# Performance work log

Hardware: AMD Instinct MI355X
Metric: run time of the kernel (lower is better)

## Reference

```python
import jax, jax.numpy as jnp
import numpy as np

RADIUS = 2                 # soft detection radius (init kwarg)
NMS_RADIUS = 2             # hardcoded in detect_keypoints: simple_nms(scores, 2)
TOP_K = 4096
TEMPERATURE = 0.1
KSIZE = 2 * RADIUS + 1     # 5
KK = KSIZE * KSIZE         # 25


def _hw_grid(dtype):
    # flatten order j = dy*KSIZE + dx ; entry = (x_off, y_off)  (torch's [:, [1,0]])
    lin = jnp.linspace(-RADIUS, RADIUS, KSIZE, dtype=dtype)
    gx, gy = jnp.meshgrid(lin, lin)  # 'xy': gx[dy,dx]=lin[dx], gy[dy,dx]=lin[dy]
    return jnp.stack([gx, gy], axis=-1).reshape(-1, 2)  # (KK, 2)


def _maxpool(x, r):
    k = 2 * r + 1
    return jax.lax.reduce_window(x, -jnp.inf, jax.lax.max,
                                 (1, 1, k, k), (1, 1, 1, 1),
                                 ((0, 0), (0, 0), (r, r), (r, r)))


def _simple_nms(scores, r):
    zeros = jnp.zeros_like(scores)
    max_mask = scores == _maxpool(scores, r)
    for _ in range(2):
        supp_mask = _maxpool(max_mask.astype(scores.dtype), r) > 0
        supp_scores = jnp.where(supp_mask, zeros, scores)
        new_max_mask = supp_scores == _maxpool(supp_scores, r)
        max_mask = max_mask | (new_max_mask & ~supp_mask)
    return jnp.where(max_mask, scores, zeros)


def _bilinear_zeros(img, xy):
    # img: (h, w); xy: (K, 2) normalized [-1,1]; align_corners=True, zero padding
    h, w = img.shape
    px = (xy[:, 0] + 1.0) * 0.5 * (w - 1)
    py = (xy[:, 1] + 1.0) * 0.5 * (h - 1)
    x0 = jnp.floor(px); y0 = jnp.floor(py)
    wx1 = px - x0; wx0 = 1.0 - wx1
    wy1 = py - y0; wy0 = 1.0 - wy1
    def tap(xi, yi, wgt):
        valid = (xi >= 0) & (xi < w) & (yi >= 0) & (yi < h)
        xc = jnp.clip(xi, 0, w - 1).astype(jnp.int32)
        yc = jnp.clip(yi, 0, h - 1).astype(jnp.int32)
        return jnp.where(valid, img[yc, xc], 0.0) * wgt
    return (tap(x0, y0, wx0 * wy0) + tap(x0 + 1, y0, wx1 * wy0)
            + tap(x0, y0 + 1, wx0 * wy1) + tap(x0 + 1, y0 + 1, wx1 * wy1))


def _dkd_forward(scores_map):
    b, c, h, w = scores_map.shape
    dtype = scores_map.dtype
    scores_nograd = jax.lax.stop_gradient(scores_map)

    nms_scores = _simple_nms(scores_nograd, NMS_RADIUS)
    # zero out border band of width RADIUS
    ybad = (jnp.arange(h) < RADIUS) | (jnp.arange(h) >= h - RADIUS)
    xbad = (jnp.arange(w) < RADIUS) | (jnp.arange(w) >= w - RADIUS)
    border = ybad[:, None] | xbad[None, :]
    nms_scores = jnp.where(border[None, None], 0.0, nms_scores)

    # top-k over flattened score map (per image)
    _, idx = jax.lax.top_k(nms_scores.reshape(b, -1), TOP_K)  # (b, K)
    ix = idx % w
    iy = idx // w

    # patch gather == unfold(scores_map) + gather, done sparsely with zero pad
    padded = jnp.pad(scores_map[:, 0], ((0, 0), (RADIUS, RADIUS), (RADIUS, RADIUS)))
    off = jnp.arange(KSIZE)
    ys = iy[:, :, None] + off[None, None, :]           # (b, K, KSIZE)
    xs = ix[:, :, None] + off[None, None, :]
    bidx = jnp.arange(b)[:, None, None, None]
    patch_scores = padded[bidx, ys[:, :, :, None], xs[:, :, None, :]]  # (b,K,KSIZE,KSIZE)
    patch_scores = patch_scores.reshape(b, TOP_K, KK)

    hw_grid = _hw_grid(dtype)                          # (KK, 2)
    max_v = jax.lax.stop_gradient(patch_scores.max(axis=-1, keepdims=True))
    x_exp = jnp.exp((patch_scores - max_v) / TEMPERATURE)   # (b,K,KK)
    x_exp_sum = x_exp.sum(axis=-1, keepdims=True)            # (b,K,1)
    xy_residual = jnp.einsum('bkp,pd->bkd', x_exp, hw_grid) / x_exp_sum  # (b,K,2)
    hw_dist2 = (((hw_grid[None, None] - xy_residual[:, :, None]) / RADIUS) ** 2).sum(-1)
    scoredispersity = (x_exp * hw_dist2).sum(-1) / x_exp_sum[..., 0]     # (b,K)

    keypoints_xy_nms = jnp.stack([ix, iy], axis=-1).astype(dtype)
    wh = jnp.array([w - 1, h - 1], dtype=dtype)
    keypoints_xy = (keypoints_xy_nms + xy_residual) / wh * 2.0 - 1.0     # (b,K,2)

    kptscore = jax.vmap(_bilinear_zeros)(scores_map[:, 0], keypoints_xy)  # (b,K)
    return keypoints_xy, kptscore, scoredispersity


def setup_inputs() -> dict:
    key = jax.random.key(0)
    scores_map = jax.random.uniform(key, (8, 1, 1024, 1024), dtype=jnp.float32)
    return {"scores_map": scores_map}


def reference(scores_map):
    # matches torch forward: (keypoints, kptscores, scoredispersitys)
    return _dkd_forward(scores_map)
```

## Files before the change

### kernel.cpp

```cpp
#include <hip/hip_runtime.h>
#include <stdint.h>

namespace {

constexpr int B = 8;
constexpr int H = 1024;
constexpr int W = 1024;
constexpr int TOPK = 4096;
constexpr int CAND_CAP = 131072;
constexpr int SEL_CAP = 16384;
constexpr int LIST_CAP = 320;
constexpr int HIST_N = 32768;
constexpr int NCHUNK = 32;
constexpr int NHB = 48;

constexpr int RROWS = 92;
constexpr int NG = 22;
constexpr int STR = 88;
constexpr int MW4 = 4;
constexpr int NSTRIP = 11;
constexpr int NUNIT = NG * NSTRIP;

constexpr int RK_ME = 256;
constexpr int RK_CH = 1024;

constexpr size_t OFF_CNT   = 0;
constexpr size_t OFF_GHIST = 4096;
constexpr size_t OFF_RANK  = OFF_GHIST + (size_t)B * HIST_N * 4;
constexpr size_t OFF_SEL   = OFF_RANK + (size_t)B * SEL_CAP * 4;
constexpr size_t OFF_TOPK  = OFF_SEL + (size_t)B * SEL_CAP * 8;
constexpr size_t OFF_CAND  = OFF_TOPK + (size_t)B * TOPK * 8;
constexpr size_t MEMSET_BYTES = OFF_RANK + (size_t)B * SEL_CAP * 4;

__device__ __forceinline__ float max5(float a, float b, float c, float d, float e) {
  return fmaxf(fmaxf(fmaxf(a, b), fmaxf(c, d)), e);
}
__device__ __forceinline__ float4 ld4(const float* p) {
  return *reinterpret_cast<const float4*>(p);
}

template <int PASS>
__device__ __forceinline__ void score_pass(
    int u, int x0, int y0, const float* __restrict__ S,
    const uint32_t* __restrict__ SUP, uint32_t* __restrict__ MA,
    uint64_t* list, uint32_t* cnt_loc, uint64_t* cand, uint32_t* cand_count, int b) {
  const int G = u % NG, s = u / NG;
  const int r0 = 2 + 8 * s;
  const int gx0 = x0 - 12 + 4 * G;
  uint32_t colm = 0;
#pragma unroll
  for (int j = 0; j < 4; ++j)
    if ((unsigned)(gx0 + j) < (unsigned)W) colm |= 1u << j;
  const int p = 4 * G - 4;
  const int pw = (p < 0) ? 0 : (p >> 5);
  const int psh = (p < 0) ? 0 : (p & 31);
  const int pls = (p < 0) ? -p : 0;

  float4 hw[5], cw[5];
  uint32_t sn[5];
#pragma unroll
  for (int k = 0; k < 12; ++k) {
    const int rr = r0 - 2 + k;
    const float* rowp = S + rr * STR + 4 * G;
    float4 d = ld4(rowp);
    float4 a = (G > 0) ? ld4(rowp - 4) : d;
    float4 e = (G < NG - 1) ? ld4(rowp + 4) : d;
    uint32_t supn = 0;
    if (PASS != 0) {
      const uint32_t* srow = SUP + rr * MW4;
      uint64_t X = (uint64_t)srow[pw] | ((uint64_t)srow[pw + 1] << 32);
      uint64_t win = pls ? (X << pls) : (X >> psh);
      if (win & 0x001u) a.x = 0.f;
      if (win & 0x002u) a.y = 0.f;
      if (win & 0x004u) a.z = 0.f;
      if (win & 0x008u) a.w = 0.f;
      if (win & 0x010u) d.x = 0.f;
      if (win & 0x020u) d.y = 0.f;
      if (win & 0x040u) d.z = 0.f;
      if (win & 0x080u) d.w = 0.f;
      if (win & 0x100u) e.x = 0.f;
      if (win & 0x200u) e.y = 0.f;
      if (win & 0x400u) e.z = 0.f;
      if (win & 0x800u) e.w = 0.f;
      supn = (uint32_t)(win >> 4) & 0xFu;
    }
    float4 hm;
    hm.x = max5(a.z, a.w, d.x, d.y, d.z);
    hm.y = max5(a.w, d.x, d.y, d.z, d.w);
    hm.z = max5(d.x, d.y, d.z, d.w, e.x);
    hm.w = max5(d.y, d.z, d.w, e.x, e.y);
    hw[k % 5] = hm;
    cw[k % 5] = d;
    sn[k % 5] = supn;
    if (k >= 4) {
      const int rq = r0 + k - 4;
      const int gy = y0 - 12 + rq;
      float4 vm;
      vm.x = max5(hw[0].x, hw[1].x, hw[2].x, hw[3].x, hw[4].x);
      vm.y = max5(hw[0].y, hw[1].y, hw[2].y, hw[3].y, hw[4].y);
      vm.z = max5(hw[0].z, hw[1].z, hw[2].z, hw[3].z, hw[4].z);
      vm.w = max5(hw[0].w, hw[1].w, hw[2].w, hw[3].w, hw[4].w);
      float4 c = cw[(k + 3) % 5];
      uint32_t nm = (uint32_t)(c.x == vm.x) | ((uint32_t)(c.y == vm.y) << 1) |
                    ((uint32_t)(c.z == vm.z) << 2) | ((uint32_t)(c.w == vm.w) << 3);
      nm &= ((unsigned)gy < (unsigned)H) ? colm : 0u;
      const int widx = rq * MW4 + (G >> 3);
      const int shift = 4 * (G & 7);
      if (PASS == 0) {
        if (nm) atomicOr(&MA[widx], nm << shift);
      } else if (PASS == 1) {
        uint32_t v = nm & ~sn[(k + 3) % 5];
        if (v) atomicOr(&MA[widx], v << shift);
      } else {
        uint32_t fin = ((MA[widx] >> shift) & 0xFu) | (nm & ~sn[(k + 3) % 5]);
        if (fin && G >= 3 && G < 19 && rq >= 12 && rq < 76 && gy >= 2 && gy < H - 2) {
#pragma unroll
          for (int j = 0; j < 4; ++j) {
            if ((fin >> j) & 1u) {
              int gx = gx0 + j;
              if (gx >= 2 && gx < W - 2) {
                float sval = S[rq * STR + 4 * G + j];
                if (sval > 0.0f) {
                  uint32_t bits = __float_as_uint(sval);
                  uint32_t flat = (uint32_t)(gy * W + gx);
                  uint64_t key = ((uint64_t)bits << 32) | (uint64_t)(0xFFFFFFFFu - flat);
                  uint32_t pos = atomicAdd(cnt_loc, 1u);
                  if (pos < (uint32_t)LIST_CAP) {
                    list[pos] = key;
                  } else {
                    uint32_t pp = atomicAdd(&cand_count[b], 1u);
                    if (pp < (uint32_t)CAND_CAP) cand[(size_t)b * CAND_CAP + pp] = key;
                  }
                }
              }
            }
          }
        }
      }
    }
  }
}

__device__ __forceinline__ void dilate_pass(int u, int x0, int y0,
                                            const uint32_t* __restrict__ MIN_,
                                            uint32_t* __restrict__ SOUT) {
  const int G = u % NG, s = u / NG;
  const int r0 = 2 + 8 * s;
  const int gx0 = x0 - 12 + 4 * G;
  uint32_t colm = 0;
#pragma unroll
  for (int j = 0; j < 4; ++j)
    if ((unsigned)(gx0 + j) < (unsigned)W) colm |= 1u << j;
  const int p = 4 * G - 2;
  const int pw = (p < 0) ? 0 : (p >> 5);
  const int psh = (p < 0) ? 0 : (p & 31);
  const int pls = (p < 0) ? -p : 0;
  uint32_t ring[5];
#pragma unroll
  for (int k = 0; k < 12; ++k) {
    const int rr = r0 - 2 + k;
    const uint32_t* srow = MIN_ + rr * MW4;
    uint64_t X = (uint64_t)srow[pw] | ((uint64_t)srow[pw + 1] << 32);
    uint64_t win = pls ? (X << pls) : (X >> psh);
    uint64_t t = win | (win >> 1) | (win >> 2) | (win >> 3) | (win >> 4);
    ring[k % 5] = (uint32_t)t & 0xFu;
    if (k >= 4) {
      const int rq = r0 + k - 4;
      const int gy = y0 - 12 + rq;
      uint32_t nib = ring[0] | ring[1] | ring[2] | ring[3] | ring[4];
      nib &= ((unsigned)gy < (unsigned)H) ? colm : 0u;
      if (nib) atomicOr(&SOUT[rq * MW4 + (G >> 3)], nib << (4 * (G & 7)));
    }
  }
}

__global__ void __launch_bounds__(256, 4) k_nms(const float* __restrict__ scores,
                                                uint64_t* __restrict__ cand,
                                                uint32_t* __restrict__ cand_count) {
  __shared__ float S[RROWS * STR];
  __shared__ uint32_t MAs[RROWS * MW4];
  __shared__ uint32_t SP1[RROWS * MW4];
  __shared__ uint32_t SP2[RROWS * MW4];
  __shared__ uint64_t list[LIST_CAP];
  __shared__ uint32_t cnt_loc, base_g;
  const int b = blockIdx.z;
  const int x0 = blockIdx.x * 64, y0 = blockIdx.y * 64;
  const int tid = threadIdx.x;
  const float* img = scores + (size_t)b * H * W;
  if (tid == 0) cnt_loc = 0;

  for (int u = tid; u < RROWS * NG; u += 256) {
    int r = u / NG, G = u % NG;
    int gy = y0 - 12 + r, gx = x0 - 12 + 4 * G;
    float4 v;
    if ((unsigned)gy < (unsigned)H && (unsigned)gx < (unsigned)W)
      v = ld4(img + (size_t)gy * W + gx);
    else
      v = make_float4(-INFINITY, -INFINITY, -INFINITY, -INFINITY);
    *reinterpret_cast<float4*>(&S[r * STR + 4 * G]) = v;
  }
  for (int i = tid; i < RROWS * MW4; i += 256) {
    MAs[i] = 0;
    SP1[i] = 0;
    SP2[i] = 0;
  }
  __syncthreads();
  if (tid < NUNIT)
    score_pass<0>(tid, x0, y0, S, nullptr, MAs, nullptr, nullptr, nullptr, nullptr, b);
  __syncthreads();
  if (tid < NUNIT) dilate_pass(tid, x0, y0, MAs, SP1);
  __syncthreads();
  if (tid < NUNIT)
    score_pass<1>(tid, x0, y0, S, SP1, MAs, nullptr, nullptr, nullptr, nullptr, b);
  __syncthreads();
  if (tid < NUNIT) dilate_pass(tid, x0, y0, MAs, SP2);
  __syncthreads();
  if (tid < NUNIT)
    score_pass<2>(tid, x0, y0, S, SP2, MAs, list, &cnt_loc, cand, cand_count, b);
  __syncthreads();
  uint32_t nblk = cnt_loc;
  uint32_t nmain = nblk < (uint32_t)LIST_CAP ? nblk : (uint32_t)LIST_CAP;
  if (tid == 0) base_g = atomicAdd(&cand_count[b], nmain);
  __syncthreads();
  uint32_t bg = base_g;
  for (uint32_t i = tid; i < nmain; i += 256) {
    uint32_t pp = bg + i;
    if (pp < (uint32_t)CAND_CAP) cand[(size_t)b * CAND_CAP + pp] = list[i];
  }
}

__global__ void __launch_bounds__(256) k_hist(const uint64_t* __restrict__ cand,
                                              const uint32_t* __restrict__ cand_count,
                                              uint32_t* __restrict__ ghist) {
  const int b = blockIdx.y;
  uint32_t n = cand_count[b];
  if (n > (uint32_t)CAND_CAP) n = CAND_CAP;
  uint32_t* gh = ghist + (size_t)b * HIST_N;
  const uint64_t* cb = cand + (size_t)b * CAND_CAP;
  const int lane = threadIdx.x & 63;
  for (uint32_t i = blockIdx.x * 256 + threadIdx.x;; i += NHB * 256) {
    bool valid = i < n;
    uint64_t act = __ballot(valid);
    if (!act) break;
    uint32_t bkt = 0;
    if (valid) bkt = (uint32_t)(cb[i] >> 47);
    uint64_t peers = act;
#pragma unroll
    for (int bit = 0; bit < 15; ++bit) {
      uint64_t bb = __ballot((bkt >> bit) & 1u);
      peers &= ((bkt >> bit) & 1u) ? bb : ~bb;
    }
    if (valid && (__ffsll((unsigned long long)peers) - 1) == lane)
      atomicAdd(&gh[bkt], (uint32_t)__popcll((unsigned long long)peers));
  }
}

__global__ void __launch_bounds__(256) k_chunksum(const uint32_t* __restrict__ ghist,
                                                  uint32_t* __restrict__ gchunk) {
  const int b = blockIdx.y, c = blockIdx.x;
  const uint32_t* gh = ghist + (size_t)b * HIST_N + c * 1024;
  uint32_t s = 0;
#pragma unroll
  for (int j = 0; j < 4; ++j) s += gh[threadIdx.x + 256 * j];
#pragma unroll
  for (int m = 1; m < 64; m <<= 1) s += __shfl_xor(s, m);
  __shared__ uint32_t red[4];
  if ((threadIdx.x & 63) == 0) red[threadIdx.x >> 6] = s;
  __syncthreads();
  if (threadIdx.x == 0) gchunk[b * NCHUNK + c] = red[0] + red[1] + red[2] + red[3];
}

__global__ void __launch_bounds__(1024) k_findthr(const uint32_t* __restrict__ ghist,
                                                  const uint32_t* __restrict__ gchunk,
                                                  uint64_t* __restrict__ thr_key) {
  __shared__ uint32_t ch[NCHUNK];
  __shared__ uint32_t h[1024];
  __shared__ int shCC;
  __shared__ uint32_t sh_above;
  const int b = blockIdx.x, t = threadIdx.x;
  if (t < NCHUNK) ch[t] = gchunk[b * NCHUNK + t];
  __syncthreads();
  if (t == 0) {
    uint32_t run = 0;
    int CC = -1;
    uint32_t above = 0;
    for (int c = NCHUNK - 1; c >= 0; --c) {
      uint32_t nrun = run + ch[c];
      if (run < (uint32_t)TOPK && nrun >= (uint32_t)TOPK) { CC = c; above = run; }
      run = nrun;
    }
    if (run < (uint32_t)TOPK) CC = -1;
    shCC = CC;
    sh_above = above;
  }
  __syncthreads();
  const int CC = shCC;
  if (CC < 0) {
    if (t == 0) thr_key[b] = 0ull;
    return;
  }
  const uint32_t above = sh_above;
  h[t] = ghist[(size_t)b * HIST_N + CC * 1024 + t];
  __syncthreads();
  for (int d = 1; d < 1024; d <<= 1) {
    uint32_t v = (t + d < 1024) ? h[t + d] : 0u;
    __syncthreads();
    h[t] += v;
    __syncthreads();
  }
  uint32_t cum = above + h[t];
  uint32_t cumn = (t + 1 < 1024) ? above + h[t + 1] : above;
  if (cum >= (uint32_t)TOPK && cumn < (uint32_t)TOPK)
    thr_key[b] = (uint64_t)(CC * 1024 + t) << 47;
}

__global__ void __launch_bounds__(1024) k_compact(const uint64_t* __restrict__ cand,
                                                  const uint32_t* __restrict__ cand_count,
                                                  const uint64_t* __restrict__ thr_key,
                                                  uint64_t* __restrict__ sel,
                                                  uint32_t* __restrict__ sel_count) {
  __shared__ uint64_t list[1024];
  __shared__ uint32_t cnt_loc;
  __shared__ uint32_t base_g;
  const int b = blockIdx.y;
  uint32_t n = cand_count[b];
  if (n > (uint32_t)CAND_CAP) n = CAND_CAP;
  const int tid = threadIdx.x;
  if (tid == 0) cnt_loc = 0;
  __syncthreads();
  uint32_t i = blockIdx.x * 1024 + tid;
  if (i < n) {
    uint64_t key = cand[(size_t)b * CAND_CAP + i];
    if (key >= thr_key[b]) {
      uint32_t pos = atomicAdd(&cnt_loc, 1u);
      list[pos] = key;
    }
  }
  __syncthreads();
  uint32_t nblk = cnt_loc;
  if (tid == 0 && nblk > 0) base_g = atomicAdd(&sel_count[b], nblk);
  __syncthreads();
  if (nblk > 0 && (uint32_t)tid < nblk) {
    uint32_t pp = base_g + tid;
    if (pp < (uint32_t)SEL_CAP) sel[(size_t)b * SEL_CAP + pp] = list[tid];
  }
}

__global__ void __launch_bounds__(RK_ME) k_rank_part(const uint64_t* __restrict__ sel,
                                                     const uint32_t* __restrict__ sel_count,
                                                     uint32_t* __restrict__ rankg) {
  __shared__ uint64_t keys[RK_CH];
  const int b = blockIdx.z;
  uint32_t n = sel_count[b];
  if (n > (uint32_t)SEL_CAP) n = SEL_CAP;
  const uint32_t me0 = blockIdx.x * RK_ME;
  const uint32_t c0 = blockIdx.y * RK_CH;
  if (me0 >= n || c0 >= n) return;
  const uint64_t* sb = sel + (size_t)b * SEL_CAP;
  uint32_t clen = n - c0;
  if (clen > (uint32_t)RK_CH) clen = RK_CH;
  for (uint32_t i = threadIdx.x; i < clen; i += RK_ME) keys[i] = sb[c0 + i];
  __syncthreads();
  const uint32_t me = me0 + threadIdx.x;
  if (me >= n) return;
  const uint64_t kme = sb[me];
  uint32_t rank = 0;
  uint32_t i = 0;
  for (; i + 8 <= clen; i += 8) {
    rank += (keys[i] > kme);
    rank += (keys[i + 1] > kme);
    rank += (keys[i + 2] > kme);
    rank += (keys[i + 3] > kme);
    rank += (keys[i + 4] > kme);
    rank += (keys[i + 5] > kme);
    rank += (keys[i + 6] > kme);
    rank += (keys[i + 7] > kme);
  }
  for (; i < clen; ++i) rank += (keys[i] > kme);
  if (rank) atomicAdd(&rankg[(size_t)b * SEL_CAP + me], rank);
}

__global__ void __launch_bounds__(256) k_scatter(const uint64_t* __restrict__ sel,
                                                 const uint32_t* __restrict__ sel_count,
                                                 const uint32_t* __restrict__ rankg,
                                                 uint64_t* __restrict__ topk) {
  const int b = blockIdx.y;
  uint32_t n = sel_count[b];
  if (n > (uint32_t)SEL_CAP) n = SEL_CAP;
  uint32_t i = blockIdx.x * 256 + threadIdx.x;
  if (i >= n) return;
  uint32_t r = rankg[(size_t)b * SEL_CAP + i];
  if (r < (uint32_t)TOPK) topk[(size_t)b * TOPK + r] = sel[(size_t)b * SEL_CAP + i];
}

__global__ void __launch_bounds__(256) k_refine(const float* __restrict__ scores,
                                                const uint64_t* __restrict__ topk,
                                                float* __restrict__ out) {
  int gid = blockIdx.x * 256 + threadIdx.x;
  int kp = gid >> 3, ln = gid & 7;
  const int b = kp / TOPK;
  const int k = kp % TOPK;
  uint64_t key = topk[(size_t)b * TOPK + k];
  uint32_t flat = 0xFFFFFFFFu - (uint32_t)(key & 0xFFFFFFFFull);
  if (flat >= (uint32_t)(H * W)) flat = 0;
  const int ix = (int)(flat % W);
  const int iy = (int)(flat / W);
  const float* img = scores + (size_t)b * H * W;

  const int nt = (ln == 0) ? 4 : 3;
  float v[4];
  float mymax = -INFINITY;
#pragma unroll
  for (int i = 0; i < 4; ++i) {
    if (i < nt) {
      int t = ln + 8 * i;
      int y = iy + t / 5 - 2, x = ix + t % 5 - 2;
      float val = ((unsigned)x < (unsigned)W && (unsigned)y < (unsigned)H)
                      ? img[(size_t)y * W + x] : 0.0f;
      v[i] = val;
      mymax = fmaxf(mymax, val);
    }
  }
#pragma unroll
  for (int m = 1; m < 8; m <<= 1) mymax = fmaxf(mymax, __shfl_xor(mymax, m));
  float e[4];
  float sum = 0.f, sx = 0.f, sy = 0.f;
#pragma unroll
  for (int i = 0; i < 4; ++i) {
    if (i < nt) {
      int t = ln + 8 * i;
      float ev = expf((v[i] - mymax) / 0.1f);
      e[i] = ev;
      sum += ev;
      sx += ev * (float)(t % 5 - 2);
      sy += ev * (float)(t / 5 - 2);
    }
  }
#pragma unroll
  for (int m = 1; m < 8; m <<= 1) {
    sum += __shfl_xor(sum, m);
    sx += __shfl_xor(sx, m);
    sy += __shfl_xor(sy, m);
  }
  float rx = sx / sum, ry = sy / sum;
  float dsp = 0.f;
#pragma unroll
  for (int i = 0; i < 4; ++i) {
    if (i < nt) {
      int t = ln + 8 * i;
      float dx = ((float)(t % 5 - 2) - rx) * 0.5f;
      float dy = ((float)(t / 5 - 2) - ry) * 0.5f;
      dsp += e[i] * (dx * dx + dy * dy);
    }
  }
#pragma unroll
  for (int m = 1; m < 8; m <<= 1) dsp += __shfl_xor(dsp, m);
  if (ln != 0) return;
  dsp /= sum;
  float kx = ((float)ix + rx) / 1023.0f * 2.0f - 1.0f;
  float ky = ((float)iy + ry) / 1023.0f * 2.0f - 1.0f;
  float px = (kx + 1.0f) * 0.5f * 1023.0f;
  float py = (ky + 1.0f) * 0.5f * 1023.0f;
  float x0f = floorf(px), y0f = floorf(py);
  float wx1 = px - x0f, wx0 = 1.0f - wx1;
  float wy1 = py - y0f, wy0 = 1.0f - wy1;
  int x0 = (int)x0f, y0 = (int)y0f;
  float sc = 0.0f;
  {
    int xs[2] = {x0, x0 + 1};
    int ys[2] = {y0, y0 + 1};
    float wxs[2] = {wx0, wx1};
    float wys[2] = {wy0, wy1};
#pragma unroll
    for (int yy = 0; yy < 2; ++yy)
#pragma unroll
      for (int xx = 0; xx < 2; ++xx) {
        int xi = xs[xx], yi = ys[yy];
        bool valid = (xi >= 0 && xi < W && yi >= 0 && yi < H);
        int xc = min(max(xi, 0), W - 1);
        int yc = min(max(yi, 0), H - 1);
        float vv = valid ? img[(size_t)yc * W + xc] : 0.0f;
        sc += vv * (wxs[xx] * wys[yy]);
      }
  }
  out[((size_t)b * TOPK + k) * 2 + 0] = kx;
  out[((size_t)b * TOPK + k) * 2 + 1] = ky;
  out[(size_t)B * TOPK * 2 + (size_t)b * TOPK + k] = sc;
  out[(size_t)B * TOPK * 3 + (size_t)b * TOPK + k] = dsp;
}

}

extern "C" void kernel_launch(void* const* d_in, const int* in_sizes, int n_in,
                              void* d_out, int out_size, void* d_ws, size_t ws_size,
                              hipStream_t stream) {
  const float* scores = (const float*)d_in[0];
  float* out = (float*)d_out;
  char* ws = (char*)d_ws;

  uint32_t* cnt = (uint32_t*)(ws + OFF_CNT);
  uint32_t* cand_count = cnt;
  uint32_t* sel_count  = cnt + 8;
  uint64_t* thr_key    = (uint64_t*)(cnt + 16);
  uint32_t* gchunk     = cnt + 256;
  uint32_t* ghist = (uint32_t*)(ws + OFF_GHIST);
  uint32_t* rankg = (uint32_t*)(ws + OFF_RANK);
  uint64_t* sel  = (uint64_t*)(ws + OFF_SEL);
  uint64_t* topk = (uint64_t*)(ws + OFF_TOPK);
  uint64_t* cand = (uint64_t*)(ws + OFF_CAND);

  hipMemsetAsync(ws + OFF_CNT, 0, MEMSET_BYTES, stream);

  k_nms<<<dim3(W / 64, H / 64, B), 256, 0, stream>>>(scores, cand, cand_count);
  k_hist<<<dim3(NHB, B), 256, 0, stream>>>(cand, cand_count, ghist);
  k_chunksum<<<dim3(NCHUNK, B), 256, 0, stream>>>(ghist, gchunk);
  k_findthr<<<B, 1024, 0, stream>>>(ghist, gchunk, thr_key);
  k_compact<<<dim3(CAND_CAP / 1024, B), 1024, 0, stream>>>(cand, cand_count, thr_key, sel, sel_count);
  k_rank_part<<<dim3(SEL_CAP / RK_ME, SEL_CAP / RK_CH, B), RK_ME, 0, stream>>>(sel, sel_count, rankg);
  k_scatter<<<dim3(SEL_CAP / 256, B), 256, 0, stream>>>(sel, sel_count, rankg, topk);
  k_refine<<<(B * TOPK * 8) / 256, 256, 0, stream>>>(scores, topk, out);
}
```

Before: 224.9 us.

## Restructure NMS masks as per-group bytes and fuse scatter into refine

Replaces the packed-bitmask, atomicOr-based NMS masks in shared memory with one byte per 4-pixel group. Suppressed scores are now zeroed directly in the tile instead of being masked again in every pass. It also merges the chunk-sum kernel into the threshold search, fuses the top-k scatter into the refine kernel, halves the selection capacity, and swaps the workspace memset for a zeroing kernel. These changes cut kernel launches and shared-memory atomics, but final candidate scores are now read from global memory, and the launch-bounds occupancy hint drops from 4 to 3 blocks per CU.

```diff
diff --git a/kernel.cpp b/kernel.cpp
--- a/kernel.cpp
+++ b/kernel.cpp
@@ -8,16 +8,14 @@
 constexpr int W = 1024;
 constexpr int TOPK = 4096;
 constexpr int CAND_CAP = 131072;
-constexpr int SEL_CAP = 16384;
+constexpr int SEL_CAP = 8192;
 constexpr int LIST_CAP = 320;
 constexpr int HIST_N = 32768;
-constexpr int NCHUNK = 32;
 constexpr int NHB = 48;
 
 constexpr int RROWS = 92;
 constexpr int NG = 22;
 constexpr int STR = 88;
-constexpr int MW4 = 4;
 constexpr int NSTRIP = 11;
 constexpr int NUNIT = NG * NSTRIP;
 
@@ -28,9 +26,8 @@
 constexpr size_t OFF_GHIST = 4096;
 constexpr size_t OFF_RANK  = OFF_GHIST + (size_t)B * HIST_N * 4;
 constexpr size_t OFF_SEL   = OFF_RANK + (size_t)B * SEL_CAP * 4;
-constexpr size_t OFF_TOPK  = OFF_SEL + (size_t)B * SEL_CAP * 8;
-constexpr size_t OFF_CAND  = OFF_TOPK + (size_t)B * TOPK * 8;
-constexpr size_t MEMSET_BYTES = OFF_RANK + (size_t)B * SEL_CAP * 4;
+constexpr size_t OFF_CAND  = OFF_SEL + (size_t)B * SEL_CAP * 8;
+constexpr size_t ZERO_BYTES = OFF_SEL;
 
 __device__ __forceinline__ float max5(float a, float b, float c, float d, float e) {
   return fmaxf(fmaxf(fmaxf(a, b), fmaxf(c, d)), e);
@@ -42,7 +39,8 @@
 template <int PASS>
 __device__ __forceinline__ void score_pass(
     int u, int x0, int y0, const float* __restrict__ S,
-    const uint32_t* __restrict__ SUP, uint32_t* __restrict__ MA,
+    const uint8_t* __restrict__ SUPb, uint8_t* __restrict__ Mb,
+    const float* __restrict__ img,
     uint64_t* list, uint32_t* cnt_loc, uint64_t* cand, uint32_t* cand_count, int b) {
   const int G = u % NG, s = u / NG;
   const int r0 = 2 + 8 * s;
@@ -51,13 +49,8 @@
 #pragma unroll
   for (int j = 0; j < 4; ++j)
     if ((unsigned)(gx0 + j) < (unsigned)W) colm |= 1u << j;
-  const int p = 4 * G - 4;
-  const int pw = (p < 0) ? 0 : (p >> 5);
-  const int psh = (p < 0) ? 0 : (p & 31);
-  const int pls = (p < 0) ? -p : 0;
 
   float4 hw[5], cw[5];
-  uint32_t sn[5];
 #pragma unroll
   for (int k = 0; k < 12; ++k) {
     const int rr = r0 - 2 + k;
@@ -65,25 +58,6 @@
     float4 d = ld4(rowp);
     float4 a = (G > 0) ? ld4(rowp - 4) : d;
     float4 e = (G < NG - 1) ? ld4(rowp + 4) : d;
-    uint32_t supn = 0;
-    if (PASS != 0) {
-      const uint32_t* srow = SUP + rr * MW4;
-      uint64_t X = (uint64_t)srow[pw] | ((uint64_t)srow[pw + 1] << 32);
-      uint64_t win = pls ? (X << pls) : (X >> psh);
-      if (win & 0x001u) a.x = 0.f;
-      if (win & 0x002u) a.y = 0.f;
-      if (win & 0x004u) a.z = 0.f;
-      if (win & 0x008u) a.w = 0.f;
-      if (win & 0x010u) d.x = 0.f;
-      if (win & 0x020u) d.y = 0.f;
-      if (win & 0x040u) d.z = 0.f;
-      if (win & 0x080u) d.w = 0.f;
-      if (win & 0x100u) e.x = 0.f;
-      if (win & 0x200u) e.y = 0.f;
-      if (win & 0x400u) e.z = 0.f;
-      if (win & 0x800u) e.w = 0.f;
-      supn = (uint32_t)(win >> 4) & 0xFu;
-    }
     float4 hm;
     hm.x = max5(a.z, a.w, d.x, d.y, d.z);
     hm.y = max5(a.w, d.x, d.y, d.z, d.w);
@@ -91,7 +65,6 @@
     hm.w = max5(d.y, d.z, d.w, e.x, e.y);
     hw[k % 5] = hm;
     cw[k % 5] = d;
-    sn[k % 5] = supn;
     if (k >= 4) {
       const int rq = r0 + k - 4;
       const int gy = y0 - 12 + rq;
@@ -104,22 +77,22 @@
       uint32_t nm = (uint32_t)(c.x == vm.x) | ((uint32_t)(c.y == vm.y) << 1) |
                     ((uint32_t)(c.z == vm.z) << 2) | ((uint32_t)(c.w == vm.w) << 3);
       nm &= ((unsigned)gy < (unsigned)H) ? colm : 0u;
-      const int widx = rq * MW4 + (G >> 3);
-      const int shift = 4 * (G & 7);
+      const int mi = G * RROWS + rq;
       if (PASS == 0) {
-        if (nm) atomicOr(&MA[widx], nm << shift);
+        Mb[mi] = (uint8_t)nm;
       } else if (PASS == 1) {
-        uint32_t v = nm & ~sn[(k + 3) % 5];
-        if (v) atomicOr(&MA[widx], v << shift);
+        uint32_t sp = SUPb[mi];
+        Mb[mi] = (uint8_t)(Mb[mi] | (nm & ~sp));
       } else {
-        uint32_t fin = ((MA[widx] >> shift) & 0xFu) | (nm & ~sn[(k + 3) % 5]);
+        uint32_t sp = SUPb[mi];
+        uint32_t fin = Mb[mi] | (nm & ~sp);
         if (fin && G >= 3 && G < 19 && rq >= 12 && rq < 76 && gy >= 2 && gy < H - 2) {
 #pragma unroll
           for (int j = 0; j < 4; ++j) {
             if ((fin >> j) & 1u) {
               int gx = gx0 + j;
               if (gx >= 2 && gx < W - 2) {
-                float sval = S[rq * STR + 4 * G + j];
+                float sval = img[(size_t)gy * W + gx];
                 if (sval > 0.0f) {
                   uint32_t bits = __float_as_uint(sval);
                   uint32_t flat = (uint32_t)(gy * W + gx);
@@ -142,8 +115,8 @@
 }
 
 __device__ __forceinline__ void dilate_pass(int u, int x0, int y0,
-                                            const uint32_t* __restrict__ MIN_,
-                                            uint32_t* __restrict__ SOUT) {
+                                            const uint8_t* __restrict__ Min,
+                                            uint8_t* __restrict__ Sout) {
   const int G = u % NG, s = u / NG;
   const int r0 = 2 + 8 * s;
   const int gx0 = x0 - 12 + 4 * G;
@@ -151,36 +124,49 @@
 #pragma unroll
   for (int j = 0; j < 4; ++j)
     if ((unsigned)(gx0 + j) < (unsigned)W) colm |= 1u << j;
-  const int p = 4 * G - 2;
-  const int pw = (p < 0) ? 0 : (p >> 5);
-  const int psh = (p < 0) ? 0 : (p & 31);
-  const int pls = (p < 0) ? -p : 0;
   uint32_t ring[5];
 #pragma unroll
   for (int k = 0; k < 12; ++k) {
     const int rr = r0 - 2 + k;
-    const uint32_t* srow = MIN_ + rr * MW4;
-    uint64_t X = (uint64_t)srow[pw] | ((uint64_t)srow[pw + 1] << 32);
-    uint64_t win = pls ? (X << pls) : (X >> psh);
-    uint64_t t = win | (win >> 1) | (win >> 2) | (win >> 3) | (win >> 4);
-    ring[k % 5] = (uint32_t)t & 0xFu;
+    uint32_t b1 = Min[G * RROWS + rr];
+    uint32_t b0 = (G > 0) ? Min[(G - 1) * RROWS + rr] : 0u;
+    uint32_t b2 = (G < NG - 1) ? Min[(G + 1) * RROWS + rr] : 0u;
+    uint32_t uu = b0 | (b1 << 4) | (b2 << 8);
+    uint32_t t = uu | (uu >> 1) | (uu >> 2) | (uu >> 3) | (uu >> 4);
+    ring[k % 5] = (t >> 2) & 0xFu;
     if (k >= 4) {
       const int rq = r0 + k - 4;
       const int gy = y0 - 12 + rq;
       uint32_t nib = ring[0] | ring[1] | ring[2] | ring[3] | ring[4];
       nib &= ((unsigned)gy < (unsigned)H) ? colm : 0u;
-      if (nib) atomicOr(&SOUT[rq * MW4 + (G >> 3)], nib << (4 * (G & 7)));
-    }
-  }
-}
-
-__global__ void __launch_bounds__(256, 4) k_nms(const float* __restrict__ scores,
+      Sout[G * RROWS + rq] = (uint8_t)nib;
+    }
+  }
+}
+
+__device__ __forceinline__ void apply_sup(int tid, float* S, const uint8_t* Sp) {
+  for (int u = tid; u < RROWS * NG; u += 256) {
+    int r = u / NG, G = u % NG;
+    uint32_t sp = Sp[G * RROWS + r];
+    if (sp) {
+      float* p = &S[r * STR + 4 * G];
+      float4 v = ld4(p);
+      if (sp & 1u) v.x = 0.f;
+      if (sp & 2u) v.y = 0.f;
+      if (sp & 4u) v.z = 0.f;
+      if (sp & 8u) v.w = 0.f;
+      *reinterpret_cast<float4*>(p) = v;
+    }
+  }
+}
+
+__global__ void __launch_bounds__(256, 3) k_nms(const float* __restrict__ scores,
                                                 uint64_t* __restrict__ cand,
                                                 uint32_t* __restrict__ cand_count) {
   __shared__ float S[RROWS * STR];
-  __shared__ uint32_t MAs[RROWS * MW4];
-  __shared__ uint32_t SP1[RROWS * MW4];
-  __shared__ uint32_t SP2[RROWS * MW4];
+  __shared__ uint8_t Mb[NG * RROWS];
+  __shared__ uint8_t Sp1[NG * RROWS];
+  __shared__ uint8_t Sp2[NG * RROWS];
   __shared__ uint64_t list[LIST_CAP];
   __shared__ uint32_t cnt_loc, base_g;
   const int b = blockIdx.z;
@@ -199,24 +185,23 @@
       v = make_float4(-INFINITY, -INFINITY, -INFINITY, -INFINITY);
     *reinterpret_cast<float4*>(&S[r * STR + 4 * G]) = v;
   }
-  for (int i = tid; i < RROWS * MW4; i += 256) {
-    MAs[i] = 0;
-    SP1[i] = 0;
-    SP2[i] = 0;
-  }
   __syncthreads();
   if (tid < NUNIT)
-    score_pass<0>(tid, x0, y0, S, nullptr, MAs, nullptr, nullptr, nullptr, nullptr, b);
-  __syncthreads();
-  if (tid < NUNIT) dilate_pass(tid, x0, y0, MAs, SP1);
+    score_pass<0>(tid, x0, y0, S, nullptr, Mb, img, nullptr, nullptr, nullptr, nullptr, b);
+  __syncthreads();
+  if (tid < NUNIT) dilate_pass(tid, x0, y0, Mb, Sp1);
+  __syncthreads();
+  apply_sup(tid, S, Sp1);
   __syncthreads();
   if (tid < NUNIT)
-    score_pass<1>(tid, x0, y0, S, SP1, MAs, nullptr, nullptr, nullptr, nullptr, b);
-  __syncthreads();
-  if (tid < NUNIT) dilate_pass(tid, x0, y0, MAs, SP2);
+    score_pass<1>(tid, x0, y0, S, Sp1, Mb, img, nullptr, nullptr, nullptr, nullptr, b);
+  __syncthreads();
+  if (tid < NUNIT) dilate_pass(tid, x0, y0, Mb, Sp2);
+  __syncthreads();
+  apply_sup(tid, S, Sp2);
   __syncthreads();
   if (tid < NUNIT)
-    score_pass<2>(tid, x0, y0, S, SP2, MAs, list, &cnt_loc, cand, cand_count, b);
+    score_pass<2>(tid, x0, y0, S, Sp2, Mb, img, list, &cnt_loc, cand, cand_count, b);
   __syncthreads();
   uint32_t nblk = cnt_loc;
   uint32_t nmain = nblk < (uint32_t)LIST_CAP ? nblk : (uint32_t)LIST_CAP;
@@ -227,6 +212,13 @@
     uint32_t pp = bg + i;
     if (pp < (uint32_t)CAND_CAP) cand[(size_t)b * CAND_CAP + pp] = list[i];
   }
+}
+
+__global__ void __launch_bounds__(256) k_zero(float4* __restrict__ p, int n4) {
+  int i = blockIdx.x * 256 + threadIdx.x;
+  const int stride = gridDim.x * 256;
+  const float4 z = make_float4(0.f, 0.f, 0.f, 0.f);
+  for (; i < n4; i += stride) p[i] = z;
 }
 
 __global__ void __launch_bounds__(256) k_hist(const uint64_t* __restrict__ cand,
@@ -255,63 +247,45 @@
   }
 }
 
-__global__ void __launch_bounds__(256) k_chunksum(const uint32_t* __restrict__ ghist,
-                                                  uint32_t* __restrict__ gchunk) {
-  const int b = blockIdx.y, c = blockIdx.x;
-  const uint32_t* gh = ghist + (size_t)b * HIST_N + c * 1024;
-  uint32_t s = 0;
-#pragma unroll
-  for (int j = 0; j < 4; ++j) s += gh[threadIdx.x + 256 * j];
-#pragma unroll
-  for (int m = 1; m < 64; m <<= 1) s += __shfl_xor(s, m);
-  __shared__ uint32_t red[4];
-  if ((threadIdx.x & 63) == 0) red[threadIdx.x >> 6] = s;
-  __syncthreads();
-  if (threadIdx.x == 0) gchunk[b * NCHUNK + c] = red[0] + red[1] + red[2] + red[3];
-}
-
 __global__ void __launch_bounds__(1024) k_findthr(const uint32_t* __restrict__ ghist,
-                                                  const uint32_t* __restrict__ gchunk,
                                                   uint64_t* __restrict__ thr_key) {
-  __shared__ uint32_t ch[NCHUNK];
-  __shared__ uint32_t h[1024];
-  __shared__ int shCC;
+  __shared__ uint32_t part[1024];
+  __shared__ int shT;
   __shared__ uint32_t sh_above;
   const int b = blockIdx.x, t = threadIdx.x;
-  if (t < NCHUNK) ch[t] = gchunk[b * NCHUNK + t];
-  __syncthreads();
-  if (t == 0) {
-    uint32_t run = 0;
-    int CC = -1;
-    uint32_t above = 0;
-    for (int c = NCHUNK - 1; c >= 0; --c) {
-      uint32_t nrun = run + ch[c];
-      if (run < (uint32_t)TOPK && nrun >= (uint32_t)TOPK) { CC = c; above = run; }
-      run = nrun;
-    }
-    if (run < (uint32_t)TOPK) CC = -1;
-    shCC = CC;
-    sh_above = above;
-  }
-  __syncthreads();
-  const int CC = shCC;
-  if (CC < 0) {
+  const uint32_t* gh = ghist + (size_t)b * HIST_N;
+  uint32_t s = 0;
+#pragma unroll 4
+  for (int i = 0; i < 32; ++i) s += gh[t * 32 + i];
+  part[t] = s;
+  if (t == 0) { shT = -1; sh_above = 0; }
+  __syncthreads();
+  for (int d = 1; d < 1024; d <<= 1) {
+    uint32_t v = (t + d < 1024) ? part[t + d] : 0u;
+    __syncthreads();
+    part[t] += v;
+    __syncthreads();
+  }
+  if (part[0] < (uint32_t)TOPK) {
     if (t == 0) thr_key[b] = 0ull;
     return;
   }
-  const uint32_t above = sh_above;
-  h[t] = ghist[(size_t)b * HIST_N + CC * 1024 + t];
-  __syncthreads();
-  for (int d = 1; d < 1024; d <<= 1) {
-    uint32_t v = (t + d < 1024) ? h[t + d] : 0u;
-    __syncthreads();
-    h[t] += v;
-    __syncthreads();
-  }
-  uint32_t cum = above + h[t];
-  uint32_t cumn = (t + 1 < 1024) ? above + h[t + 1] : above;
-  if (cum >= (uint32_t)TOPK && cumn < (uint32_t)TOPK)
-    thr_key[b] = (uint64_t)(CC * 1024 + t) << 47;
+  {
+    uint32_t mine = part[t];
+    uint32_t nxt = (t + 1 < 1024) ? part[t + 1] : 0u;
+    if (mine >= (uint32_t)TOPK && nxt < (uint32_t)TOPK) { shT = t; sh_above = nxt; }
+  }
+  __syncthreads();
+  if (t == 0) {
+    const int T = shT;
+    uint32_t run = sh_above;
+    int bkt = T * 32;
+    for (int i = 31; i >= 0; --i) {
+      run += gh[T * 32 + i];
+      if (run >= (uint32_t)TOPK) { bkt = T * 32 + i; break; }
+    }
+    thr_key[b] = (uint64_t)bkt << 47;
+  }
 }
 
 __global__ void __launch_bounds__(1024) k_compact(const uint64_t* __restrict__ cand,
@@ -380,27 +354,20 @@
   if (rank) atomicAdd(&rankg[(size_t)b * SEL_CAP + me], rank);
 }
 
-__global__ void __launch_bounds__(256) k_scatter(const uint64_t* __restrict__ sel,
-                                                 const uint32_t* __restrict__ sel_count,
-                                                 const uint32_t* __restrict__ rankg,
-                                                 uint64_t* __restrict__ topk) {
+__global__ void __launch_bounds__(256) k_refine(const float* __restrict__ scores,
+                                                const uint64_t* __restrict__ sel,
+                                                const uint32_t* __restrict__ sel_count,
+                                                const uint32_t* __restrict__ rankg,
+                                                float* __restrict__ out) {
   const int b = blockIdx.y;
   uint32_t n = sel_count[b];
   if (n > (uint32_t)SEL_CAP) n = SEL_CAP;
-  uint32_t i = blockIdx.x * 256 + threadIdx.x;
-  if (i >= n) return;
-  uint32_t r = rankg[(size_t)b * SEL_CAP + i];
-  if (r < (uint32_t)TOPK) topk[(size_t)b * TOPK + r] = sel[(size_t)b * SEL_CAP + i];
-}
-
-__global__ void __launch_bounds__(256) k_refine(const float* __restrict__ scores,
-                                                const uint64_t* __restrict__ topk,
-                                                float* __restrict__ out) {
   int gid = blockIdx.x * 256 + threadIdx.x;
-  int kp = gid >> 3, ln = gid & 7;
-  const int b = kp / TOPK;
-  const int k = kp % TOPK;
-  uint64_t key = topk[(size_t)b * TOPK + k];
+  int si = gid >> 3, ln = gid & 7;
+  if ((uint32_t)si >= n) return;
+  uint32_t r = rankg[(size_t)b * SEL_CAP + si];
+  if (r >= (uint32_t)TOPK) return;
+  uint64_t key = sel[(size_t)b * SEL_CAP + si];
   uint32_t flat = 0xFFFFFFFFu - (uint32_t)(key & 0xFFFFFFFFull);
   if (flat >= (uint32_t)(H * W)) flat = 0;
   const int ix = (int)(flat % W);
@@ -483,10 +450,10 @@
         sc += vv * (wxs[xx] * wys[yy]);
       }
   }
-  out[((size_t)b * TOPK + k) * 2 + 0] = kx;
-  out[((size_t)b * TOPK + k) * 2 + 1] = ky;
-  out[(size_t)B * TOPK * 2 + (size_t)b * TOPK + k] = sc;
-  out[(size_t)B * TOPK * 3 + (size_t)b * TOPK + k] = dsp;
+  out[((size_t)b * TOPK + r) * 2 + 0] = kx;
+  out[((size_t)b * TOPK + r) * 2 + 1] = ky;
+  out[(size_t)B * TOPK * 2 + (size_t)b * TOPK + r] = sc;
+  out[(size_t)B * TOPK * 3 + (size_t)b * TOPK + r] = dsp;
 }
 
 }
@@ -502,21 +469,16 @@
   uint32_t* cand_count = cnt;
   uint32_t* sel_count  = cnt + 8;
   uint64_t* thr_key    = (uint64_t*)(cnt + 16);
-  uint32_t* gchunk     = cnt + 256;
   uint32_t* ghist = (uint32_t*)(ws + OFF_GHIST);
   uint32_t* rankg = (uint32_t*)(ws + OFF_RANK);
   uint64_t* sel  = (uint64_t*)(ws + OFF_SEL);
-  uint64_t* topk = (uint64_t*)(ws + OFF_TOPK);
   uint64_t* cand = (uint64_t*)(ws + OFF_CAND);
 
-  hipMemsetAsync(ws + OFF_CNT, 0, MEMSET_BYTES, stream);
-
+  k_zero<<<256, 256, 0, stream>>>((float4*)ws, (int)(ZERO_BYTES / 16));
   k_nms<<<dim3(W / 64, H / 64, B), 256, 0, stream>>>(scores, cand, cand_count);
   k_hist<<<dim3(NHB, B), 256, 0, stream>>>(cand, cand_count, ghist);
-  k_chunksum<<<dim3(NCHUNK, B), 256, 0, stream>>>(ghist, gchunk);
-  k_findthr<<<B, 1024, 0, stream>>>(ghist, gchunk, thr_key);
+  k_findthr<<<B, 1024, 0, stream>>>(ghist, thr_key);
   k_compact<<<dim3(CAND_CAP / 1024, B), 1024, 0, stream>>>(cand, cand_count, thr_key, sel, sel_count);
   k_rank_part<<<dim3(SEL_CAP / RK_ME, SEL_CAP / RK_CH, B), RK_ME, 0, stream>>>(sel, sel_count, rankg);
-  k_scatter<<<dim3(SEL_CAP / 256, B), 256, 0, stream>>>(sel, sel_count, rankg, topk);
-  k_refine<<<(B * TOPK * 8) / 256, 256, 0, stream>>>(scores, topk, out);
-}
+  k_refine<<<dim3(SEL_CAP * 8 / 256, B), 256, 0, stream>>>(scores, sel, sel_count, rankg, out);
+}
```

Result: slower. 236.1 us (+5.0%).
